# Kernel tuning notes

Measured on AMD Instinct MI355X. Metric: run time of the kernel, lower is better.

The kernel has to match this reference:

```python
import jax, jax.numpy as jnp
import numpy as np

# ---- configuration (matches init_kwargs) ----
IH, IW, IC, OC = 32, 32, 8, 16
KH = KW = 3
STRIDE = (1, 1)
PAD = (1, 1)
DIL = (1, 1)
P = 5                       # num_gp_pts per GP neuron
I_DIM = IC * KH * KW        # 72 = kernel_input_size
OH = (IH + 2 * PAD[0] - DIL[0] * (KH - 1) - 1) // STRIDE[0] + 1
OW = (IW + 2 * PAD[1] - DIL[1] * (KW - 1) - 1) // STRIDE[1] + 1
JITTER = 1e-4


def setup_inputs() -> dict:
    key = jax.random.key(0)
    k1, k2, k3, k4, k5 = jax.random.split(key, 5)
    N = 8
    x_mean = jax.random.normal(k1, (N, IH, IW, IC), jnp.float32)
    # variances must be positive
    x_var = 0.1 + 0.9 * jax.random.uniform(k2, (N, IH, IW, IC), jnp.float32)
    # inducing inputs: spread on [-1,1] with small perturbation (well-conditioned K)
    base = jnp.linspace(-1.0, 1.0, P, dtype=jnp.float32)
    z = base[None, None, :] + 0.05 * jax.random.normal(k3, (OC, I_DIM, P), jnp.float32)
    h = jax.random.normal(k4, (OC, I_DIM, P), jnp.float32)      # inducing outputs
    raw_l = jax.random.uniform(k5, (OC, I_DIM), jnp.float32)    # pre-softplus lengthscale
    return {"x_mean": x_mean, "x_var": x_var, "z": z, "h": h, "raw_l": raw_l}


def im2col(img):
    """[N,IH,IW,C] NHWC -> [N*L, C*KH*KW], torch.nn.Unfold ordering (channel slowest)."""
    x = jnp.transpose(img, (0, 3, 1, 2))  # NCHW, matches the torch transposes
    patches = jax.lax.conv_general_dilated_patches(
        x, (KH, KW), STRIDE, [(PAD[0], PAD[0]), (PAD[1], PAD[1])], rhs_dilation=DIL
    )  # [N, C*KH*KW, OH, OW], feature dim channel-major like torch unfold
    Nb = patches.shape[0]
    return patches.reshape(Nb, I_DIM, OH * OW).transpose(0, 2, 1).reshape(Nb * OH * OW, I_DIM)


def gp_layer(mu, s2, z, h, raw_l):
    """GP-neuron (KAN-style) moment propagation.
    mu, s2: [R, I]; z, h: [O, I, P]; raw_l: [O, I].
    Per neuron (o,i): SE kernel k(a,b)=exp(-(a-b)^2/(2 l^2)), unit signal variance.
    Under x_i ~ N(mu_i, s2_i):
      q_p   = sqrt(l^2/(l^2+s2)) * exp(-(mu-z_p)^2 / (2 (l^2+s2)))   (expected kernel)
      mean  = q . K^{-1} h
      var   = 1 - q . K^{-1} q
    Layer output (KAN sum over inputs): y_o = sum_i f_oi(x_i).
    """
    l2 = jax.nn.softplus(raw_l) ** 2                                  # [O,I]
    dz = z[:, :, :, None] - z[:, :, None, :]                          # [O,I,P,P]
    K = jnp.exp(-0.5 * dz**2 / l2[:, :, None, None]) + JITTER * jnp.eye(P, dtype=mu.dtype)
    Kinv = jnp.linalg.inv(K)                                          # [O,I,P,P] (tiny)
    alpha = jnp.einsum('oipq,oiq->oip', Kinv, h)                      # [O,I,P]

    d = l2[None, :, :, None] + s2[:, None, :, None]                   # [R,O,I,1]
    diff = mu[:, None, :, None] - z[None]                             # [R,O,I,P]
    q = jnp.sqrt(l2[None, :, :, None] / d) * jnp.exp(-0.5 * diff**2 / d)  # [R,O,I,P]

    out_mean = jnp.einsum('roip,oip->ro', q, alpha)                   # [R,O]
    qK = jnp.einsum('roip,oipq->roiq', q, Kinv)                       # [R,O,I,P]
    qKq = jnp.einsum('roiq,roiq->ro', qK, q)                          # [R,O]
    # sum_i (k(x,x) - q K^{-1} q) with k(x,x)=1 -> I - sum_i qKq_i
    out_var = jnp.maximum(jnp.asarray(mu.shape[1], mu.dtype) - qKq, 1e-6)
    return out_mean, out_var


def reference(x_mean, x_var, z, h, raw_l):
    N = x_mean.shape[0]
    mu = im2col(x_mean)                  # [N*L, I]
    s2 = im2col(x_var)                   # [N*L, I]
    m, v = gp_layer(mu, s2, z, h, raw_l)
    # col2im: [N*L, OC] -> [N, OH, OW, OC]
    return m.reshape(N, OH, OW, OC), v.reshape(N, OH, OW, OC)
```

## Files before the change

### kernel.cpp

```cpp
#include <hip/hip_runtime.h>
#include <math.h>

#define OC_N   16
#define I_DIM  72
#define PN     5
#define NEU    (OC_N * I_DIM)
#define NF     32
#define RTOT   8192
#define OUT_HALF (RTOT * OC_N)

#if __has_builtin(__builtin_amdgcn_rcpf)
#define RCPF(x) __builtin_amdgcn_rcpf(x)
#else
#define RCPF(x) (1.0f / (x))
#endif
#if __has_builtin(__builtin_amdgcn_exp2f)
#define EXP2F(x) __builtin_amdgcn_exp2f(x)
#else
#define EXP2F(x) exp2f(x)
#endif


__global__ void gp_prep_kernel(const float* __restrict__ zin,
                               const float* __restrict__ hin,
                               const float* __restrict__ rlin,
                               float* __restrict__ nr) {
  int idx = blockIdx.x * blockDim.x + threadIdx.x;
  if (idx >= NEU) return;
  double x = (double)rlin[idx];
  double sp = (x > 30.0) ? x : log1p(exp(x));
  double l2 = sp * sp;
  double zz[PN], hh[PN];
#pragma unroll
  for (int p = 0; p < PN; ++p) {
    zz[p] = (double)zin[idx * PN + p];
    hh[p] = (double)hin[idx * PN + p];
  }
  double A[PN][PN], B[PN][PN];
#pragma unroll
  for (int p = 0; p < PN; ++p) {
#pragma unroll
    for (int q = 0; q < PN; ++q) {
      double dz = zz[p] - zz[q];
      A[p][q] = exp(-0.5 * dz * dz / l2);
      B[p][q] = (p == q) ? 1.0 : 0.0;
    }
  }
#pragma unroll
  for (int p = 0; p < PN; ++p) A[p][p] += 1e-4;

  for (int c = 0; c < PN; ++c) {
    double pivinv = 1.0 / A[c][c];
    for (int j = 0; j < PN; ++j) { A[c][j] *= pivinv; B[c][j] *= pivinv; }
    for (int r = 0; r < PN; ++r) {
      if (r == c) continue;
      double f = A[r][c];
      for (int j = 0; j < PN; ++j) { A[r][j] -= f * A[c][j]; B[r][j] -= f * B[c][j]; }
    }
  }
  double alpha[PN];
#pragma unroll
  for (int p = 0; p < PN; ++p) {
    double s = 0.0;
    for (int q = 0; q < PN; ++q) s += B[p][q] * hh[q];
    alpha[p] = s;
  }
  float* o = nr + idx * NF;
  o[0] = (float)l2;
  o[1] = 0.0f;
#pragma unroll
  for (int p = 0; p < PN; ++p) {
    o[2 + p]  = (float)zz[p];
    o[7 + p]  = (float)alpha[p];
    o[12 + p] = (float)B[p][p];
  }
  int j = 17;
  for (int p = 0; p < PN; ++p)
    for (int q = p + 1; q < PN; ++q) o[j++] = (float)(2.0 * B[p][q]);
  o[27] = o[28] = o[29] = o[30] = o[31] = 0.0f;
}

__global__ __launch_bounds__(256) void gp_main_kernel(
    const float* __restrict__ xm, const float* __restrict__ xv,
    const float* __restrict__ nr, float* __restrict__ out) {
  const int o = blockIdx.y;
  const int r = blockIdx.x * 256 + threadIdx.x;
  const int n  = r >> 10;
  const int pix = r & 1023;
  const int oh = pix >> 5;
  const int ow = pix & 31;
  const float* nb = nr + o * (I_DIM * NF);

  float mean_acc = 0.0f;
  float qkq_acc  = 0.0f;

#pragma unroll 1
  for (int k = 0; k < 9; ++k) {
    const int kh = k / 3;
    const int kw = k - kh * 3;
    const int ih = oh + kh - 1;
    const int iw = ow + kw - 1;
    const bool vld = ((unsigned)ih < 32u) & ((unsigned)iw < 32u);
    float mu[8], s2[8];
    if (vld) {
      const int base = ((n * 32 + ih) * 32 + iw) * 8;
      const float4 a0 = *(const float4*)(xm + base);
      const float4 a1 = *(const float4*)(xm + base + 4);
      const float4 b0 = *(const float4*)(xv + base);
      const float4 b1 = *(const float4*)(xv + base + 4);
      mu[0]=a0.x; mu[1]=a0.y; mu[2]=a0.z; mu[3]=a0.w;
      mu[4]=a1.x; mu[5]=a1.y; mu[6]=a1.z; mu[7]=a1.w;
      s2[0]=b0.x; s2[1]=b0.y; s2[2]=b0.z; s2[3]=b0.w;
      s2[4]=b1.x; s2[5]=b1.y; s2[6]=b1.z; s2[7]=b1.w;
    } else {
#pragma unroll
      for (int c = 0; c < 8; ++c) { mu[c] = 0.0f; s2[c] = 0.0f; }
    }
#pragma unroll
    for (int c = 0; c < 8; ++c) {
      const float* p = nb + (c * 9 + k) * NF;
      const float l2    = p[0];
      const float d     = l2 + s2[c];
      const float inv_d = RCPF(d);
      const float coef2 = l2 * inv_d;
      const float coef  = sqrtf(coef2);
      const float el    = -0.72134752044f * inv_d;
      const float m     = mu[c];
      const float d0 = m - p[2];
      const float d1 = m - p[3];
      const float d2 = m - p[4];
      const float d3 = m - p[5];
      const float d4 = m - p[6];
      const float u0 = EXP2F(el * d0 * d0);
      const float u1 = EXP2F(el * d1 * d1);
      const float u2 = EXP2F(el * d2 * d2);
      const float u3 = EXP2F(el * d3 * d3);
      const float u4 = EXP2F(el * d4 * d4);
      const float dotA =
          fmaf(u0, p[7], fmaf(u1, p[8], fmaf(u2, p[9], fmaf(u3, p[10], u4 * p[11]))));
      const float t0 = fmaf(p[12], u0, fmaf(p[17], u1, fmaf(p[18], u2, fmaf(p[19], u3, p[20] * u4))));
      const float t1 = fmaf(p[13], u1, fmaf(p[21], u2, fmaf(p[22], u3, p[23] * u4)));
      const float t2 = fmaf(p[14], u2, fmaf(p[24], u3, p[25] * u4));
      const float t3 = fmaf(p[15], u3, p[26] * u4);
      const float t4 = p[16] * u4;
      const float quad =
          fmaf(u0, t0, fmaf(u1, t1, fmaf(u2, t2, fmaf(u3, t3, u4 * t4))));
      mean_acc = fmaf(coef, dotA, mean_acc);
      qkq_acc  = fmaf(coef2, quad, qkq_acc);
    }
  }
  const int oi = r * OC_N + o;
  out[oi] = mean_acc;
  out[OUT_HALF + oi] = fmaxf(72.0f - qkq_acc, 1e-6f);
}

extern "C" void kernel_launch(void* const* d_in, const int* in_sizes, int n_in,
                              void* d_out, int out_size, void* d_ws, size_t ws_size,
                              hipStream_t stream) {
  const float* xm = (const float*)d_in[0];
  const float* xv = (const float*)d_in[1];
  const float* z  = (const float*)d_in[2];
  const float* h  = (const float*)d_in[3];
  const float* rl = (const float*)d_in[4];
  float* out = (float*)d_out;
  float* nr  = (float*)d_ws;

  gp_prep_kernel<<<dim3((NEU + 255) / 256), dim3(256), 0, stream>>>(z, h, rl, nr);

  dim3 grid(RTOT / 256, OC_N);
  gp_main_kernel<<<grid, dim3(256), 0, stream>>>(xm, xv, nr, out);
}
```

Baseline: 107.9 us.

## Split main kernel over kernel rows with atomics; float32 prep with smaller blocks

The main kernel's 9-tap loop is split across a third grid dimension, one kernel row per block. Partial sums are combined with atomicAdd into zeroed workspace buffers, and a new final kernel applies the variance clamp. This triples the parallelism to fill more CUs, at the cost of a memset, an extra launch and atomic traffic. The prep kernel moves from double to float with full unrolling and 64-thread blocks, which removes slow FP64 work and risks accuracy in the 5x5 inverse.

```diff
diff --git a/kernel.cpp b/kernel.cpp
--- a/kernel.cpp
+++ b/kernel.cpp
@@ -21,69 +21,78 @@
 #endif
 
 
-__global__ void gp_prep_kernel(const float* __restrict__ zin,
-                               const float* __restrict__ hin,
-                               const float* __restrict__ rlin,
-                               float* __restrict__ nr) {
+__global__ __launch_bounds__(64) void gp_prep_kernel(
+    const float* __restrict__ zin, const float* __restrict__ hin,
+    const float* __restrict__ rlin, float* __restrict__ nr) {
   int idx = blockIdx.x * blockDim.x + threadIdx.x;
   if (idx >= NEU) return;
-  double x = (double)rlin[idx];
-  double sp = (x > 30.0) ? x : log1p(exp(x));
-  double l2 = sp * sp;
-  double zz[PN], hh[PN];
+  float x = rlin[idx];
+  float sp = (x > 20.0f) ? x : log1pf(expf(x));
+  float l2 = sp * sp;
+  float inv_l2 = 1.0f / l2;
+  float zz[PN], hh[PN];
 #pragma unroll
   for (int p = 0; p < PN; ++p) {
-    zz[p] = (double)zin[idx * PN + p];
-    hh[p] = (double)hin[idx * PN + p];
+    zz[p] = zin[idx * PN + p];
+    hh[p] = hin[idx * PN + p];
   }
-  double A[PN][PN], B[PN][PN];
+  float A[PN][PN], B[PN][PN];
 #pragma unroll
   for (int p = 0; p < PN; ++p) {
 #pragma unroll
     for (int q = 0; q < PN; ++q) {
-      double dz = zz[p] - zz[q];
-      A[p][q] = exp(-0.5 * dz * dz / l2);
-      B[p][q] = (p == q) ? 1.0 : 0.0;
+      float dz = zz[p] - zz[q];
+      A[p][q] = expf(-0.5f * dz * dz * inv_l2);
+      B[p][q] = (p == q) ? 1.0f : 0.0f;
     }
   }
 #pragma unroll
-  for (int p = 0; p < PN; ++p) A[p][p] += 1e-4;
+  for (int p = 0; p < PN; ++p) A[p][p] += 1e-4f;
 
+#pragma unroll
   for (int c = 0; c < PN; ++c) {
-    double pivinv = 1.0 / A[c][c];
+    float pivinv = 1.0f / A[c][c];
+#pragma unroll
     for (int j = 0; j < PN; ++j) { A[c][j] *= pivinv; B[c][j] *= pivinv; }
+#pragma unroll
     for (int r = 0; r < PN; ++r) {
       if (r == c) continue;
-      double f = A[r][c];
+      float f = A[r][c];
+#pragma unroll
       for (int j = 0; j < PN; ++j) { A[r][j] -= f * A[c][j]; B[r][j] -= f * B[c][j]; }
     }
   }
-  double alpha[PN];
+  float alpha[PN];
 #pragma unroll
   for (int p = 0; p < PN; ++p) {
-    double s = 0.0;
+    float s = 0.0f;
+#pragma unroll
     for (int q = 0; q < PN; ++q) s += B[p][q] * hh[q];
     alpha[p] = s;
   }
   float* o = nr + idx * NF;
-  o[0] = (float)l2;
+  o[0] = l2;
   o[1] = 0.0f;
 #pragma unroll
   for (int p = 0; p < PN; ++p) {
-    o[2 + p]  = (float)zz[p];
-    o[7 + p]  = (float)alpha[p];
-    o[12 + p] = (float)B[p][p];
+    o[2 + p]  = zz[p];
+    o[7 + p]  = alpha[p];
+    o[12 + p] = B[p][p];
   }
   int j = 17;
+#pragma unroll
   for (int p = 0; p < PN; ++p)
-    for (int q = p + 1; q < PN; ++q) o[j++] = (float)(2.0 * B[p][q]);
+#pragma unroll
+    for (int q = p + 1; q < PN; ++q) o[j++] = 2.0f * B[p][q];
   o[27] = o[28] = o[29] = o[30] = o[31] = 0.0f;
 }
 
 __global__ __launch_bounds__(256) void gp_main_kernel(
     const float* __restrict__ xm, const float* __restrict__ xv,
-    const float* __restrict__ nr, float* __restrict__ out) {
-  const int o = blockIdx.y;
+    const float* __restrict__ nr,
+    float* __restrict__ mean_buf, float* __restrict__ qkq_buf) {
+  const int o   = blockIdx.y;
+  const int seg = blockIdx.z;
   const int r = blockIdx.x * 256 + threadIdx.x;
   const int n  = r >> 10;
   const int pix = r & 1023;
@@ -94,13 +103,14 @@
   float mean_acc = 0.0f;
   float qkq_acc  = 0.0f;
 
+  const int ih = oh + seg - 1;
+  const bool hvld = ((unsigned)ih < 32u);
+
 #pragma unroll 1
-  for (int k = 0; k < 9; ++k) {
-    const int kh = k / 3;
-    const int kw = k - kh * 3;
-    const int ih = oh + kh - 1;
+  for (int kw = 0; kw < 3; ++kw) {
+    const int k = seg * 3 + kw;
     const int iw = ow + kw - 1;
-    const bool vld = ((unsigned)ih < 32u) & ((unsigned)iw < 32u);
+    const bool vld = hvld & ((unsigned)iw < 32u);
     float mu[8], s2[8];
     if (vld) {
       const int base = ((n * 32 + ih) * 32 + iw) * 8;
@@ -150,8 +160,16 @@
     }
   }
   const int oi = r * OC_N + o;
-  out[oi] = mean_acc;
-  out[OUT_HALF + oi] = fmaxf(72.0f - qkq_acc, 1e-6f);
+  atomicAdd(mean_buf + oi, mean_acc);
+  atomicAdd(qkq_buf + oi, qkq_acc);
+}
+
+__global__ __launch_bounds__(256) void gp_final_kernel(
+    const float* __restrict__ mean_buf, const float* __restrict__ qkq_buf,
+    float* __restrict__ out) {
+  const int i = blockIdx.x * 256 + threadIdx.x;
+  out[i] = mean_buf[i];
+  out[OUT_HALF + i] = fmaxf(72.0f - qkq_buf[i], 1e-6f);
 }
 
 extern "C" void kernel_launch(void* const* d_in, const int* in_sizes, int n_in,
@@ -163,10 +181,17 @@
   const float* h  = (const float*)d_in[3];
   const float* rl = (const float*)d_in[4];
   float* out = (float*)d_out;
-  float* nr  = (float*)d_ws;
 
-  gp_prep_kernel<<<dim3((NEU + 255) / 256), dim3(256), 0, stream>>>(z, h, rl, nr);
+  float* nr       = (float*)d_ws;
+  float* mean_buf = (float*)((char*)d_ws + NEU * NF * 4);
+  float* qkq_buf  = mean_buf + OUT_HALF;
 
-  dim3 grid(RTOT / 256, OC_N);
-  gp_main_kernel<<<grid, dim3(256), 0, stream>>>(xm, xv, nr, out);
+  hipMemsetAsync(mean_buf, 0, 2 * OUT_HALF * sizeof(float), stream);
+
+  gp_prep_kernel<<<dim3((NEU + 63) / 64), dim3(64), 0, stream>>>(z, h, rl, nr);
+
+  dim3 grid(RTOT / 256, OC_N, 3);
+  gp_main_kernel<<<grid, dim3(256), 0, stream>>>(xm, xv, nr, mean_buf, qkq_buf);
+
+  gp_final_kernel<<<dim3(OUT_HALF / 256), dim3(256), 0, stream>>>(mean_buf, qkq_buf, out);
 }
```

After: 115.9 us. 1.07x slower.
